# Performance work log

Hardware: AMD Instinct MI355X
Metric: run time of the kernel (lower is better)

The kernel has to match this reference:

```python
import jax, jax.numpy as jnp
import numpy as np

ALPHA = 0.2  # leaky relu slope
NEG = -1e9


def setup_inputs() -> dict:
    key = jax.random.key(0)
    ks = jax.random.split(key, 8)
    B, N, F_IN, H, HID, OUT = 2, 4096, 512, 4, 128, 64
    x = jax.random.normal(ks[0], (B, N, F_IN), dtype=jnp.float32)
    adj = jax.random.randint(ks[1], (B, N, N), 0, 2, dtype=jnp.int32)
    s_in = float(np.sqrt(2.0 / (F_IN + HID)))
    W_heads = jax.random.normal(ks[2], (H, HID, F_IN), dtype=jnp.float32) * s_in
    a1_heads = jax.random.normal(ks[3], (H, HID), dtype=jnp.float32) * 0.1
    a2_heads = jax.random.normal(ks[4], (H, HID), dtype=jnp.float32) * 0.1
    s_out = float(np.sqrt(2.0 / (H * HID + OUT)))
    W_out = jax.random.normal(ks[5], (OUT, H * HID), dtype=jnp.float32) * s_out
    a1_out = jax.random.normal(ks[6], (OUT,), dtype=jnp.float32) * 0.1
    a2_out = jax.random.normal(ks[7], (OUT,), dtype=jnp.float32) * 0.1
    return {"x": x, "adj": adj, "W_heads": W_heads, "a1_heads": a1_heads,
            "a2_heads": a2_heads, "W_out": W_out, "a1_out": a1_out, "a2_out": a2_out}


def _gat_layer(x, adj, W, a1, a2, concat):
    # x: [B,N,F], W: [O,F], a1/a2: [O]
    h = jnp.einsum('bnf,of->bno', x, W)            # [B,N,O]
    f1 = jnp.einsum('bno,o->bn', h, a1)            # [B,N]
    f2 = jnp.einsum('bno,o->bn', h, a2)            # [B,N]
    e = f1[:, :, None] + f2[:, None, :]            # [B,N,N] additive scores
    e = jnp.where(e > 0, e, ALPHA * e)             # leaky relu
    e = jnp.where(adj == 0, NEG, e)                # adjacency mask
    att = jax.nn.softmax(e, axis=2)
    h_prime = jnp.einsum('bnm,bmo->bno', att, h)
    return jax.nn.elu(h_prime) if concat else h_prime


def reference(x, adj, W_heads, a1_heads, a2_heads, W_out, a1_out, a2_out):
    H = W_heads.shape[0]
    heads = [_gat_layer(x, adj, W_heads[i], a1_heads[i], a2_heads[i], True)
             for i in range(H)]
    x_cat = jnp.concatenate(heads, axis=2)         # [B,N,H*HID]
    return _gat_layer(x_cat, adj, W_out, a1_out, a2_out, False)
```

## Files before the change

### kernel.cpp

```cpp
#include <hip/hip_runtime.h>

#define TB 2
#define TN 4096
#define TH 4
#define THID 128
#define TOUT 64
#define NW 128

using f4    = __attribute__((ext_vector_type(4))) float;
using s16x8 = __attribute__((ext_vector_type(8))) short;
using s16x4 = __attribute__((ext_vector_type(4))) short;
using u32x4 = __attribute__((ext_vector_type(4))) unsigned;

static __device__ __forceinline__ short f2bf(float f){
  unsigned u = __float_as_uint(f);
  unsigned r = u + 0x7FFFu + ((u >> 16) & 1u);
  return (short)(r >> 16);
}
static __device__ __forceinline__ float bf2f(short s){
  return __uint_as_float(((unsigned)(unsigned short)s) << 16);
}
static __device__ __forceinline__ unsigned encf(float f){
  unsigned u = __float_as_uint(f);
  return (u & 0x80000000u) ? ~u : (u | 0x80000000u);
}
static __device__ __forceinline__ float decf(unsigned u){
  unsigned v = (u & 0x80000000u) ? (u & 0x7FFFFFFFu) : ~u;
  return __uint_as_float(v);
}
static __device__ __forceinline__ void gll16(const void* g, void* l){
  __builtin_amdgcn_global_load_lds((const __attribute__((address_space(1))) unsigned int*)g,
                                   (__attribute__((address_space(3))) unsigned int*)l, 16, 0, 0);
}
static __device__ __forceinline__ f4 mfma_bf16(s16x8 a, s16x8 b, f4 c){
  return __builtin_amdgcn_mfma_f32_16x16x32_bf16(a, b, c, 0, 0, 0);
}

__global__ void k_pack(const int* __restrict__ adj, unsigned* __restrict__ adjp,
                       unsigned* __restrict__ mx){
  if (blockIdx.x == 0 && threadIdx.x < 16) mx[threadIdx.x] = 0;
  int t = blockIdx.x * 256 + threadIdx.x;
  const int4* p = (const int4*)adj + (size_t)t * 8;
  unsigned m = 0;
#pragma unroll
  for (int i = 0; i < 8; ++i){
    int4 v = p[i];
    m |= (v.x != 0 ? 1u : 0u) << (i*4+0);
    m |= (v.y != 0 ? 1u : 0u) << (i*4+1);
    m |= (v.z != 0 ? 1u : 0u) << (i*4+2);
    m |= (v.w != 0 ? 1u : 0u) << (i*4+3);
  }
  adjp[t] = m;
}

__global__ void k_split(const float* __restrict__ x, short* __restrict__ hi, short* __restrict__ lo){
  int t = blockIdx.x * 256 + threadIdx.x;
  f4 v = ((const f4*)x)[t];
  s16x4 h, l;
#pragma unroll
  for (int e = 0; e < 4; ++e){
    short hb = f2bf(v[e]);
    h[e] = hb;
    l[e] = f2bf(v[e] - bf2f(hb));
  }
  ((s16x4*)hi)[t] = h;
  ((s16x4*)lo)[t] = l;
}
__global__ void k_cvt(const float* __restrict__ x, short* __restrict__ o){
  int t = blockIdx.x * 256 + threadIdx.x;
  f4 v = ((const f4*)x)[t];
  s16x4 h;
#pragma unroll
  for (int e = 0; e < 4; ++e) h[e] = f2bf(v[e]);
  ((s16x4*)o)[t] = h;
}

__global__ __launch_bounds__(512, 2) void k_gemm1(
    const short* __restrict__ xh, const short* __restrict__ xl,
    const short* __restrict__ wh, const short* __restrict__ wl,
    const float* __restrict__ a1h, const float* __restrict__ a2h,
    short* __restrict__ hTb, float* __restrict__ f1g,
    float* __restrict__ Qa, float* __restrict__ Sa, unsigned* __restrict__ mx){
  __shared__ short tiles[2][4][8192];
  __shared__ float red[2][128][2];
  __shared__ float bmx[2];
  int tid = threadIdx.x, lane = tid & 63, w = tid >> 6;
  int kgrp = lane >> 4, li = lane & 15;
  int nblk = blockIdx.x >> 6, mblk = blockIdx.x & 63;
  int n0 = nblk * 128, m0 = mblk * 128;
  int wn = w >> 2, wm = w & 3;
  const f4 fz = {0.f, 0.f, 0.f, 0.f};
  f4 acc[4][2];
#pragma unroll
  for (int i = 0; i < 4; ++i)
#pragma unroll
    for (int j = 0; j < 2; ++j) acc[i][j] = fz;

#pragma unroll
  for (int tno = 0; tno < 4; ++tno){
    const short* gb = (tno==0 ? wh : tno==1 ? wl : tno==2 ? xh : xl);
    int r0 = (tno < 2) ? n0 : m0;
#pragma unroll
    for (int i = 0; i < 2; ++i){
      int s = (i*8 + w)*64 + lane;
      int row = s >> 3, c = s & 7, cs = c ^ (row & 7);
      gll16(gb + (size_t)(r0 + row)*512 + cs*8, (char*)tiles[0][tno] + (i*8+w)*1024);
    }
  }
  asm volatile("s_waitcnt vmcnt(0)" ::: "memory");
  __syncthreads();

  for (int kt = 0; kt < 8; ++kt){
    int cur = kt & 1;
    if (kt < 7){
      int k0 = (kt+1) * 64;
#pragma unroll
      for (int tno = 0; tno < 4; ++tno){
        const short* gb = (tno==0 ? wh : tno==1 ? wl : tno==2 ? xh : xl);
        int r0 = (tno < 2) ? n0 : m0;
#pragma unroll
        for (int i = 0; i < 2; ++i){
          int s = (i*8 + w)*64 + lane;
          int row = s >> 3, c = s & 7, cs = c ^ (row & 7);
          gll16(gb + (size_t)(r0 + row)*512 + k0 + cs*8, (char*)tiles[cur^1][tno] + (i*8+w)*1024);
        }
      }
    }
    const char* t0 = (const char*)tiles[cur][0];
    const char* t1 = (const char*)tiles[cur][1];
    const char* t2 = (const char*)tiles[cur][2];
    const char* t3 = (const char*)tiles[cur][3];
#pragma unroll
    for (int ks = 0; ks < 2; ++ks){
      int ck = ks*4 + kgrp;
      s16x8 ah[4], al[4], bh[2], bl[2];
#pragma unroll
      for (int fn = 0; fn < 4; ++fn){
        int row = wn*64 + fn*16 + li;
        int off = row*128 + ((ck ^ (row & 7)) << 4);
        ah[fn] = *(const s16x8*)(t0 + off);
        al[fn] = *(const s16x8*)(t1 + off);
      }
#pragma unroll
      for (int fm = 0; fm < 2; ++fm){
        int row = wm*32 + fm*16 + li;
        int off = row*128 + ((ck ^ (row & 7)) << 4);
        bh[fm] = *(const s16x8*)(t2 + off);
        bl[fm] = *(const s16x8*)(t3 + off);
      }
#pragma unroll
      for (int fn = 0; fn < 4; ++fn)
#pragma unroll
        for (int fm = 0; fm < 2; ++fm)
          acc[fn][fm] = mfma_bf16(ah[fn], bh[fm], acc[fn][fm]);
#pragma unroll
      for (int fn = 0; fn < 4; ++fn)
#pragma unroll
        for (int fm = 0; fm < 2; ++fm)
          acc[fn][fm] = mfma_bf16(ah[fn], bl[fm], acc[fn][fm]);
#pragma unroll
      for (int fn = 0; fn < 4; ++fn)
#pragma unroll
        for (int fm = 0; fm < 2; ++fm)
          acc[fn][fm] = mfma_bf16(al[fn], bh[fm], acc[fn][fm]);
    }
    asm volatile("s_waitcnt vmcnt(0)" ::: "memory");
    __syncthreads();
  }
  int head = nblk;
#pragma unroll
  for (int fn = 0; fn < 4; ++fn){
#pragma unroll
    for (int fm = 0; fm < 2; ++fm){
#pragma unroll
      for (int r = 0; r < 4; ++r){
        int nout = n0 + wn*64 + fn*16 + kgrp*4 + r;
        int m = m0 + wm*32 + fm*16 + li;
        int b = m >> 12, n = m & 4095;
        int hid = nout & 127;
        size_t idx = ((size_t)((b*TH + head)*THID + hid))*TN + n;
        hTb[idx] = f2bf(acc[fn][fm][r]);
      }
    }
  }
  const float* a1p = a1h + head*THID;
  const float* a2p = a2h + head*THID;
  float s1[2] = {0.f, 0.f}, s2[2] = {0.f, 0.f};
#pragma unroll
  for (int fn = 0; fn < 4; ++fn)
#pragma unroll
    for (int r = 0; r < 4; ++r){
      int row = wn*64 + fn*16 + kgrp*4 + r;
      float w1 = a1p[row], w2 = a2p[row];
#pragma unroll
      for (int fm = 0; fm < 2; ++fm){
        s1[fm] = fmaf(acc[fn][fm][r], w1, s1[fm]);
        s2[fm] = fmaf(acc[fn][fm][r], w2, s2[fm]);
      }
    }
#pragma unroll
  for (int fm = 0; fm < 2; ++fm){
    s1[fm] += __shfl_xor(s1[fm], 16); s1[fm] += __shfl_xor(s1[fm], 32);
    s2[fm] += __shfl_xor(s2[fm], 16); s2[fm] += __shfl_xor(s2[fm], 32);
  }
  if (kgrp == 0){
#pragma unroll
    for (int fm = 0; fm < 2; ++fm){
      int col = wm*32 + fm*16 + li;
      red[wn][col][0] = s1[fm];
      red[wn][col][1] = s2[fm];
    }
  }
  __syncthreads();
  if (tid < 128){
    float f1v = red[0][tid][0] + red[1][tid][0];
    float f2v = red[0][tid][1] + red[1][tid][1];
    int m = m0 + tid, b = m >> 12, n = m & 4095;
    int idx = (b*TH + head)*TN + n;
    f1g[idx] = f1v;
    Qa[idx] = expf(f2v);
    Sa[idx] = expf(0.2f*f2v);
    float wmx = f2v;
#pragma unroll
    for (int d = 1; d < 64; d <<= 1) wmx = fmaxf(wmx, __shfl_xor(wmx, d));
    if ((tid & 63) == 0) bmx[tid >> 6] = wmx;
  }
  __syncthreads();
  if (tid == 0){
    int b = m0 >> 12;
    atomicMax(&mx[b*TH + head], encf(fmaxf(bmx[0], bmx[1])));
  }
}

__global__ __launch_bounds__(256, 4) void k_attn1(
    const short* __restrict__ hTb, const float* __restrict__ f1,
    const float* __restrict__ Qa, const float* __restrict__ Sa,
    const unsigned* __restrict__ adjp, const unsigned* __restrict__ mx,
    short* __restrict__ part, float* __restrict__ sums){
  __shared__ short tile[2][8192];
  __shared__ float Qs[1024], Ss[1024];
  int tid = threadIdx.x, lane = tid & 63, w = tid >> 6;
  int kgrp = lane >> 4, li = lane & 15;
  int bid = blockIdx.x;
  int js = bid >> 8, b = (bid >> 7) & 1, h = (bid >> 5) & 3, rblk = bid & 31;
  int bh = b*TH + h;
  int jbase = js * 1024;
  const short* hbase = hTb + ((size_t)bh*THID)*TN;

  gll16(Qa + (size_t)bh*TN + jbase + w*256 + lane*4, (char*)Qs + w*1024);
  gll16(Sa + (size_t)bh*TN + jbase + w*256 + lane*4, (char*)Ss + w*1024);
#pragma unroll
  for (int i = 0; i < 4; ++i){
    int s = (i*4 + w)*64 + lane;
    int row = s >> 3, c = s & 7, cs = c ^ (row & 7);
    gll16(hbase + (size_t)row*TN + jbase + cs*8, (char*)tile[0] + (i*4+w)*1024);
  }
  int r0 = rblk*128 + w*32;
  float Pv[2], Rv[2];
  int rowa[2];
  float mf = decf(mx[bh]);
#pragma unroll
  for (int rf = 0; rf < 2; ++rf){
    int row = r0 + rf*16 + li;
    rowa[rf] = row;
    float f1v = f1[bh*TN + row];
    float e = f1v + mf;
    float m = e > 0.f ? e : 0.2f*e;
    Pv[rf] = expf(f1v - m);
    Rv[rf] = expf(0.2f*f1v - m);
  }
  const f4 fz = {0.f,0.f,0.f,0.f};
  f4 acc[2][8];
#pragma unroll
  for (int i = 0; i < 2; ++i)
#pragma unroll
    for (int j = 0; j < 8; ++j) acc[i][j] = fz;
  f4 accs[2] = {fz, fz};
  s16x8 ones;
#pragma unroll
  for (int e = 0; e < 8; ++e) ones[e] = (short)0x3F80;

  uint2 awc[2], awn[2];
#pragma unroll
  for (int rf = 0; rf < 2; ++rf)
    awc[rf] = *(const uint2*)&adjp[(size_t)(b*TN + rowa[rf])*NW + (jbase >> 5)];

  asm volatile("s_waitcnt vmcnt(0)" ::: "memory");
  __syncthreads();

  for (int jt = 0; jt < 16; ++jt){
    int cur = jt & 1;
    if (jt < 15){
      int jg = jbase + (jt+1)*64;
#pragma unroll
      for (int i = 0; i < 4; ++i){
        int s = (i*4 + w)*64 + lane;
        int row = s >> 3, c = s & 7, cs = c ^ (row & 7);
        gll16(hbase + (size_t)row*TN + jg + cs*8, (char*)tile[cur^1] + (i*4+w)*1024);
      }
    }
    int jn = jt < 15 ? jt+1 : jt;
#pragma unroll
    for (int rf = 0; rf < 2; ++rf)
      awn[rf] = *(const uint2*)&adjp[(size_t)(b*TN + rowa[rf])*NW + ((jbase + jn*64) >> 5)];
    int j0 = jt*64;
    const char* tp = (const char*)tile[cur];
#pragma unroll
    for (int ks = 0; ks < 2; ++ks){
      int jloc = j0 + ks*32 + kgrp*8;
      float qv[8], sv[8];
      *(f4*)&qv[0] = *(const f4*)&Qs[jloc];
      *(f4*)&qv[4] = *(const f4*)&Qs[jloc+4];
      *(f4*)&sv[0] = *(const f4*)&Ss[jloc];
      *(f4*)&sv[4] = *(const f4*)&Ss[jloc+4];
      s16x8 af[2];
#pragma unroll
      for (int rf = 0; rf < 2; ++rf){
        unsigned word = ks ? awc[rf].y : awc[rf].x;
        unsigned byt = (word >> (kgrp*8)) & 0xFFu;
        float P = Pv[rf], R = Rv[rf];
        u32x4 pw;
#pragma unroll
        for (int pe = 0; pe < 4; ++pe){
          float va = fmaxf(P*qv[2*pe],   R*sv[2*pe]);
          float vb = fmaxf(P*qv[2*pe+1], R*sv[2*pe+1]);
          va = (byt & (1u << (2*pe)))   ? va : 0.f;
          vb = (byt & (1u << (2*pe+1))) ? vb : 0.f;
          unsigned ua = __float_as_uint(va) + 0x8000u;
          unsigned ub = __float_as_uint(vb) + 0x8000u;
          pw[pe] = __builtin_amdgcn_perm(ub, ua, 0x07060302);
        }
        af[rf] = __builtin_bit_cast(s16x8, pw);
      }
      accs[0] = mfma_bf16(af[0], ones, accs[0]);
      accs[1] = mfma_bf16(af[1], ones, accs[1]);
#pragma unroll
      for (int cf = 0; cf < 8; ++cf){
        int col = cf*16 + li;
        int off = col*128 + (((ks*4 + kgrp) ^ (col & 7)) << 4);
        s16x8 bfr = *(const s16x8*)(tp + off);
        acc[0][cf] = mfma_bf16(af[0], bfr, acc[0][cf]);
        acc[1][cf] = mfma_bf16(af[1], bfr, acc[1][cf]);
      }
    }
    asm volatile("s_waitcnt vmcnt(0)" ::: "memory");
    __syncthreads();
    awc[0] = awn[0]; awc[1] = awn[1];
  }
  int sl = js*8 + bh;
  if (li == 0){
#pragma unroll
    for (int rf = 0; rf < 2; ++rf)
#pragma unroll
      for (int r = 0; r < 4; ++r)
        sums[(size_t)sl*TN + r0 + rf*16 + kgrp*4 + r] = accs[rf][r];
  }
#pragma unroll
  for (int rf = 0; rf < 2; ++rf)
#pragma unroll
    for (int cf = 0; cf < 8; ++cf)
#pragma unroll
      for (int r = 0; r < 4; ++r){
        int row = r0 + rf*16 + kgrp*4 + r;
        int hid = cf*16 + li;
        part[((size_t)sl*TN + row)*THID + hid] = f2bf(acc[rf][cf][r]);
      }
}

__global__ void k_comb1(const short* __restrict__ part, const float* __restrict__ sums,
                        short* __restrict__ xcat){
  int t = blockIdx.x*256 + threadIdx.x;
  int hid8 = t & 15, n = (t >> 4) & 4095, h = (t >> 16) & 3, b = t >> 18;
  int bh = b*TH + h;
  float a[8] = {0,0,0,0,0,0,0,0};
  float s = 0.f;
#pragma unroll
  for (int js = 0; js < 4; ++js){
    size_t rowoff = (size_t)(js*8 + bh)*TN + n;
    s16x8 pv = *(const s16x8*)(part + rowoff*THID + hid8*8);
#pragma unroll
    for (int e = 0; e < 8; ++e) a[e] += bf2f(pv[e]);
    s += sums[rowoff];
  }
  float inv = 1.f / s;
  s16x8 o;
#pragma unroll
  for (int e = 0; e < 8; ++e){
    float x = a[e] * inv;
    o[e] = f2bf(x > 0.f ? x : expm1f(x));
  }
  *(s16x8*)(xcat + ((size_t)(b*TN + n))*512 + h*128 + hid8*8) = o;
}

__global__ __launch_bounds__(128) void k_gemm2(
    const short* __restrict__ xcat, const short* __restrict__ wo,
    const float* __restrict__ a1o, const float* __restrict__ a2o,
    short* __restrict__ h2T, float* __restrict__ f1o,
    float* __restrict__ Q2, float* __restrict__ S2, unsigned* __restrict__ mx2){
  int tid = threadIdx.x, lane = tid & 63, w = tid >> 6;
  int kgrp = lane >> 4, li = lane & 15;
  int m0 = blockIdx.x * 32;
  const f4 fz = {0.f,0.f,0.f,0.f};
  f4 acc[4] = {fz, fz, fz, fz};
  int rowA = m0 + w*16 + li;
  for (int kt = 0; kt < 16; ++kt){
    int k = kt*32 + kgrp*8;
    s16x8 a = *(const s16x8*)(xcat + (size_t)rowA*512 + k);
#pragma unroll
    for (int cf = 0; cf < 4; ++cf){
      int col = cf*16 + li;
      s16x8 bfr = *(const s16x8*)(wo + (size_t)col*512 + k);
      acc[cf] = mfma_bf16(a, bfr, acc[cf]);
    }
  }
  float p1[4] = {0,0,0,0}, p2[4] = {0,0,0,0};
#pragma unroll
  for (int cf = 0; cf < 4; ++cf){
    int o = cf*16 + li;
    float w1 = a1o[o], w2 = a2o[o];
#pragma unroll
    for (int r = 0; r < 4; ++r){
      p1[r] = fmaf(acc[cf][r], w1, p1[r]);
      p2[r] = fmaf(acc[cf][r], w2, p2[r]);
    }
  }
#pragma unroll
  for (int r = 0; r < 4; ++r){
#pragma unroll
    for (int d = 1; d < 16; d <<= 1){
      p1[r] += __shfl_xor(p1[r], d);
      p2[r] += __shfl_xor(p2[r], d);
    }
  }
#pragma unroll
  for (int cf = 0; cf < 4; ++cf)
#pragma unroll
    for (int r = 0; r < 4; ++r){
      int row = m0 + w*16 + kgrp*4 + r;
      int o = cf*16 + li;
      int b = row >> 12, n = row & 4095;
      h2T[((size_t)(b*TOUT + o))*TN + n] = f2bf(acc[cf][r]);
    }
  if (li == 0){
#pragma unroll
    for (int r = 0; r < 4; ++r){
      int row = m0 + w*16 + kgrp*4 + r;
      f1o[row] = p1[r];
      Q2[row] = expf(p2[r]);
      S2[row] = expf(0.2f*p2[r]);
    }
  }
  float m2 = fmaxf(fmaxf(p2[0], p2[1]), fmaxf(p2[2], p2[3]));
  m2 = fmaxf(m2, __shfl_xor(m2, 16));
  m2 = fmaxf(m2, __shfl_xor(m2, 32));
  __shared__ float bm[2];
  if (lane == 0) bm[w] = m2;
  __syncthreads();
  if (tid == 0) atomicMax(&mx2[m0 >> 12], encf(fmaxf(bm[0], bm[1])));
}

__global__ __launch_bounds__(256, 4) void k_attn2(
    const short* __restrict__ h2T, const float* __restrict__ f1o,
    const float* __restrict__ Q2, const float* __restrict__ S2,
    const unsigned* __restrict__ adjp, const unsigned* __restrict__ mx2,
    float* __restrict__ part, float* __restrict__ sums){
  __shared__ short tile[2][4096];
  __shared__ float Qs[512], Ss[512];
  int tid = threadIdx.x, lane = tid & 63, w = tid >> 6;
  int kgrp = lane >> 4, li = lane & 15;
  int bid = blockIdx.x;
  int js = bid >> 7, b = (bid >> 6) & 1, rblk = bid & 63;
  int jbase = js * 512;
  const short* hbase = h2T + (size_t)b*TOUT*TN;

  if (w < 2) gll16(Q2 + (size_t)b*TN + jbase + w*256 + lane*4, (char*)Qs + w*1024);
  else       gll16(S2 + (size_t)b*TN + jbase + (w-2)*256 + lane*4, (char*)Ss + (w-2)*1024);
#pragma unroll
  for (int i = 0; i < 2; ++i){
    int s = (i*4 + w)*64 + lane;
    int row = s >> 3, c = s & 7, cs = c ^ (row & 7);
    gll16(hbase + (size_t)row*TN + jbase + cs*8, (char*)tile[0] + (i*4+w)*1024);
  }
  int r0 = rblk*64 + w*16;
  int rowa = r0 + li;
  float mf = decf(mx2[b]);
  float f1v = f1o[b*TN + rowa];
  float e0 = f1v + mf;
  float m0v = e0 > 0.f ? e0 : 0.2f*e0;
  float Pv = expf(f1v - m0v);
  float Rv = expf(0.2f*f1v - m0v);
  const f4 fz = {0.f,0.f,0.f,0.f};
  f4 acc[4] = {fz, fz, fz, fz};
  f4 accs = fz;
  s16x8 ones;
#pragma unroll
  for (int e = 0; e < 8; ++e) ones[e] = (short)0x3F80;

  uint2 awc, awn;
  awc = *(const uint2*)&adjp[(size_t)(b*TN + rowa)*NW + (jbase >> 5)];

  asm volatile("s_waitcnt vmcnt(0)" ::: "memory");
  __syncthreads();

  for (int jt = 0; jt < 8; ++jt){
    int cur = jt & 1;
    if (jt < 7){
      int jg = jbase + (jt+1)*64;
#pragma unroll
      for (int i = 0; i < 2; ++i){
        int s = (i*4 + w)*64 + lane;
        int row = s >> 3, c = s & 7, cs = c ^ (row & 7);
        gll16(hbase + (size_t)row*TN + jg + cs*8, (char*)tile[cur^1] + (i*4+w)*1024);
      }
    }
    int jn = jt < 7 ? jt+1 : jt;
    awn = *(const uint2*)&adjp[(size_t)(b*TN + rowa)*NW + ((jbase + jn*64) >> 5)];
    int j0 = jt*64;
    const char* tp = (const char*)tile[cur];
#pragma unroll
    for (int ks = 0; ks < 2; ++ks){
      int jloc = j0 + ks*32 + kgrp*8;
      float qv[8], sv[8];
      *(f4*)&qv[0] = *(const f4*)&Qs[jloc];
      *(f4*)&qv[4] = *(const f4*)&Qs[jloc+4];
      *(f4*)&sv[0] = *(const f4*)&Ss[jloc];
      *(f4*)&sv[4] = *(const f4*)&Ss[jloc+4];
      unsigned word = ks ? awc.y : awc.x;
      unsigned byt = (word >> (kgrp*8)) & 0xFFu;
      u32x4 pw;
#pragma unroll
      for (int pe = 0; pe < 4; ++pe){
        float va = fmaxf(Pv*qv[2*pe],   Rv*sv[2*pe]);
        float vb = fmaxf(Pv*qv[2*pe+1], Rv*sv[2*pe+1]);
        va = (byt & (1u << (2*pe)))   ? va : 0.f;
        vb = (byt & (1u << (2*pe+1))) ? vb : 0.f;
        unsigned ua = __float_as_uint(va) + 0x8000u;
        unsigned ub = __float_as_uint(vb) + 0x8000u;
        pw[pe] = __builtin_amdgcn_perm(ub, ua, 0x07060302);
      }
      s16x8 af = __builtin_bit_cast(s16x8, pw);
      accs = mfma_bf16(af, ones, accs);
#pragma unroll
      for (int cf = 0; cf < 4; ++cf){
        int col = cf*16 + li;
        int off = col*128 + (((ks*4 + kgrp) ^ (col & 7)) << 4);
        s16x8 bfr = *(const s16x8*)(tp + off);
        acc[cf] = mfma_bf16(af, bfr, acc[cf]);
      }
    }
    asm volatile("s_waitcnt vmcnt(0)" ::: "memory");
    __syncthreads();
    awc = awn;
  }
  int sl = js*2 + b;
  if (li == 0){
#pragma unroll
    for (int r = 0; r < 4; ++r)
      sums[(size_t)sl*TN + r0 + kgrp*4 + r] = accs[r];
  }
#pragma unroll
  for (int cf = 0; cf < 4; ++cf)
#pragma unroll
    for (int r = 0; r < 4; ++r){
      int row = r0 + kgrp*4 + r;
      int o = cf*16 + li;
      part[((size_t)sl*TN + row)*TOUT + o] = acc[cf][r];
    }
}

__global__ void k_comb2(const float* __restrict__ part, const float* __restrict__ sums,
                        float* __restrict__ out){
  int t = blockIdx.x*256 + threadIdx.x;
  int o4 = t & 15, n = (t >> 4) & 4095, b = t >> 16;
  f4 a = {0.f,0.f,0.f,0.f};
  float s = 0.f;
#pragma unroll
  for (int js = 0; js < 8; ++js){
    int sl = js*2 + b;
    a += ((const f4*)part)[((size_t)sl*TN + n)*16 + o4];
    s += sums[(size_t)sl*TN + n];
  }
  f4 r = a / s;
  ((f4*)out)[((size_t)(b*TN + n))*16 + o4] = r;
}

extern "C" void kernel_launch(void* const* d_in, const int* in_sizes, int n_in,
                              void* d_out, int out_size, void* d_ws, size_t ws_size,
                              hipStream_t stream) {
  (void)in_sizes; (void)n_in; (void)out_size; (void)ws_size;
  const float* x       = (const float*)d_in[0];
  const int*   adj     = (const int*)d_in[1];
  const float* W_heads = (const float*)d_in[2];
  const float* a1h     = (const float*)d_in[3];
  const float* a2h     = (const float*)d_in[4];
  const float* W_out   = (const float*)d_in[5];
  const float* a1o     = (const float*)d_in[6];
  const float* a2o     = (const float*)d_in[7];

  char* p = (char*)d_ws;
  auto alloc = [&](size_t sz){ char* r = p; p += (sz + 255) & ~(size_t)255; return r; };
  unsigned* adjp  = (unsigned*) alloc(4ull*1048576);
  short*    wo    = (short*)    alloc(2ull*32768);
  short*    hTb   = (short*)    alloc(2ull*4194304);
  float*    f1    = (float*)    alloc(4ull*32768);
  float*    Qa    = (float*)    alloc(4ull*32768);
  float*    Sa    = (float*)    alloc(4ull*32768);
  unsigned* mx    = (unsigned*) alloc(4ull*16);
  short*    xcat  = (short*)    alloc(2ull*4194304);
  float*    f1o   = (float*)    alloc(4ull*8192);
  float*    Q2    = (float*)    alloc(4ull*8192);
  float*    S2    = (float*)    alloc(4ull*8192);
  short*    h2T   = (short*)    alloc(2ull*524288);
  float*    sums1 = (float*)    alloc(4ull*131072);
  float*    sums2 = (float*)    alloc(4ull*65536);
  char* A = alloc(33554432ull);
  short* xh   = (short*)A;
  short* xl   = (short*)(A + 8388608);
  short* part1 = (short*)A;
  char* Bu = alloc(16777216ull);
  short* wh = (short*)Bu;
  short* wl = (short*)(Bu + 524288);
  float* part2 = (float*)Bu;

  k_pack <<<4096, 256, 0, stream>>>(adj, adjp, mx);
  k_split<<<4096, 256, 0, stream>>>(x, xh, xl);
  k_split<<<256, 256, 0, stream>>>(W_heads, wh, wl);
  k_cvt  <<<32, 256, 0, stream>>>(W_out, wo);
  k_gemm1<<<256, 512, 0, stream>>>(xh, xl, wh, wl, a1h, a2h, hTb, f1, Qa, Sa, mx);
  k_attn1<<<1024, 256, 0, stream>>>(hTb, f1, Qa, Sa, adjp, mx, part1, sums1);
  k_comb1<<<2048, 256, 0, stream>>>(part1, sums1, xcat);
  k_gemm2<<<256, 128, 0, stream>>>(xcat, wo, a1o, a2o, h2T, f1o, Q2, S2, mx + 8);
  k_attn2<<<1024, 256, 0, stream>>>(h2T, f1o, Q2, S2, adjp, mx + 8, part2, sums2);
  k_comb2<<<512, 256, 0, stream>>>(part2, sums2, (float*)d_out);
}
```

Before: 154.5 us.

## Transpose packed adjacency and deepen attention pipelines to four LDS stages

The packed adjacency bitmask is now stored transposed (word-major, node-minor), so each attention tile's mask bits can be bulk-loaded into LDS with global_load_lds alongside the feature tile. Both attention kernels move from a double-buffered loop with a full vmcnt(0) wait and barrier per step to a four-buffer ring with three tiles in flight and partial vmcnt waits. The second-layer attention now covers 1024 columns per block with half the blocks, so the final combine reduces over fewer splits. Occupancy hints drop to fit the larger LDS footprint, and the pack kernel's global reads become strided across rows, which may cost some bandwidth.

```diff
diff --git a/kernel.cpp b/kernel.cpp
--- a/kernel.cpp
+++ b/kernel.cpp
@@ -36,11 +36,12 @@
   return __builtin_amdgcn_mfma_f32_16x16x32_bf16(a, b, c, 0, 0, 0);
 }
 
-__global__ void k_pack(const int* __restrict__ adj, unsigned* __restrict__ adjp,
+__global__ void k_pack(const int* __restrict__ adj, unsigned* __restrict__ adjT,
                        unsigned* __restrict__ mx){
   if (blockIdx.x == 0 && threadIdx.x < 16) mx[threadIdx.x] = 0;
   int t = blockIdx.x * 256 + threadIdx.x;
-  const int4* p = (const int4*)adj + (size_t)t * 8;
+  int n = t & 4095, w = (t >> 12) & 127, b = t >> 19;
+  const int4* p = (const int4*)(adj + ((size_t)(b*TN + n))*TN + w*32);
   unsigned m = 0;
 #pragma unroll
   for (int i = 0; i < 8; ++i){
@@ -50,7 +51,7 @@
     m |= (v.z != 0 ? 1u : 0u) << (i*4+2);
     m |= (v.w != 0 ? 1u : 0u) << (i*4+3);
   }
-  adjp[t] = m;
+  adjT[((size_t)(b*NW + w))*TN + n] = m;
 }
 
 __global__ void k_split(const float* __restrict__ x, short* __restrict__ hi, short* __restrict__ lo){
@@ -232,37 +233,50 @@
   }
 }
 
-__global__ __launch_bounds__(256, 4) void k_attn1(
+__global__ __launch_bounds__(256, 2) void k_attn1(
     const short* __restrict__ hTb, const float* __restrict__ f1,
     const float* __restrict__ Qa, const float* __restrict__ Sa,
-    const unsigned* __restrict__ adjp, const unsigned* __restrict__ mx,
+    const unsigned* __restrict__ adjT, const unsigned* __restrict__ mx,
     short* __restrict__ part, float* __restrict__ sums){
-  __shared__ short tile[2][8192];
+  __shared__ short tile[4][8192];
   __shared__ float Qs[1024], Ss[1024];
+  __shared__ unsigned abuf[4][256];
   int tid = threadIdx.x, lane = tid & 63, w = tid >> 6;
   int kgrp = lane >> 4, li = lane & 15;
   int bid = blockIdx.x;
   int js = bid >> 8, b = (bid >> 7) & 1, h = (bid >> 5) & 3, rblk = bid & 31;
   int bh = b*TH + h;
   int jbase = js * 1024;
+  int r0b = rblk * 128;
   const short* hbase = hTb + ((size_t)bh*THID)*TN;
-
-  gll16(Qa + (size_t)bh*TN + jbase + w*256 + lane*4, (char*)Qs + w*1024);
-  gll16(Sa + (size_t)bh*TN + jbase + w*256 + lane*4, (char*)Ss + w*1024);
-#pragma unroll
-  for (int i = 0; i < 4; ++i){
-    int s = (i*4 + w)*64 + lane;
-    int row = s >> 3, c = s & 7, cs = c ^ (row & 7);
-    gll16(hbase + (size_t)row*TN + jbase + cs*8, (char*)tile[0] + (i*4+w)*1024);
-  }
-  int r0 = rblk*128 + w*32;
+  const float* Qrow = Qa + (size_t)bh*TN + jbase;
+  const float* Srow = Sa + (size_t)bh*TN + jbase;
+
+  auto STAGE = [&](int t){
+    int jg = jbase + t*64;
+    char* dst = (char*)tile[t & 3];
+#pragma unroll
+    for (int i = 0; i < 4; ++i){
+      int s = (i*4 + w)*64 + lane;
+      int row = s >> 3, c = s & 7, cs = c ^ (row & 7);
+      gll16(hbase + (size_t)row*TN + jg + cs*8, dst + (i*4+w)*1024);
+    }
+    int w0 = jg >> 5;
+    gll16(adjT + (size_t)(b*NW + w0 + (lane>>5))*TN + r0b + (lane&31)*4, (char*)abuf[t & 3]);
+  };
+
+  gll16(Qrow + w*256 + lane*4, (char*)Qs + w*1024);
+  gll16(Srow + w*256 + lane*4, (char*)Ss + w*1024);
+  STAGE(0); STAGE(1); STAGE(2);
+
+  int r0 = r0b + w*32;
   float Pv[2], Rv[2];
-  int rowa[2];
+  int lrow[2];
   float mf = decf(mx[bh]);
 #pragma unroll
   for (int rf = 0; rf < 2; ++rf){
     int row = r0 + rf*16 + li;
-    rowa[rf] = row;
+    lrow[rf] = w*32 + rf*16 + li;
     float f1v = f1[bh*TN + row];
     float e = f1v + mf;
     float m = e > 0.f ? e : 0.2f*e;
@@ -280,31 +294,23 @@
 #pragma unroll
   for (int e = 0; e < 8; ++e) ones[e] = (short)0x3F80;
 
-  uint2 awc[2], awn[2];
-#pragma unroll
-  for (int rf = 0; rf < 2; ++rf)
-    awc[rf] = *(const uint2*)&adjp[(size_t)(b*TN + rowa[rf])*NW + (jbase >> 5)];
-
-  asm volatile("s_waitcnt vmcnt(0)" ::: "memory");
-  __syncthreads();
-
   for (int jt = 0; jt < 16; ++jt){
-    int cur = jt & 1;
-    if (jt < 15){
-      int jg = jbase + (jt+1)*64;
-#pragma unroll
-      for (int i = 0; i < 4; ++i){
-        int s = (i*4 + w)*64 + lane;
-        int row = s >> 3, c = s & 7, cs = c ^ (row & 7);
-        gll16(hbase + (size_t)row*TN + jg + cs*8, (char*)tile[cur^1] + (i*4+w)*1024);
-      }
-    }
-    int jn = jt < 15 ? jt+1 : jt;
-#pragma unroll
-    for (int rf = 0; rf < 2; ++rf)
-      awn[rf] = *(const uint2*)&adjp[(size_t)(b*TN + rowa[rf])*NW + ((jbase + jn*64) >> 5)];
+    if (jt < 14)       asm volatile("s_waitcnt vmcnt(10)" ::: "memory");
+    else if (jt == 14) asm volatile("s_waitcnt vmcnt(5)" ::: "memory");
+    else               asm volatile("s_waitcnt vmcnt(0)" ::: "memory");
+    __builtin_amdgcn_s_barrier();
+    __builtin_amdgcn_sched_barrier(0);
+    if (jt < 13) STAGE(jt + 3);
+
     int j0 = jt*64;
-    const char* tp = (const char*)tile[cur];
+    const char* tp = (const char*)tile[jt & 3];
+    const unsigned* ab = abuf[jt & 3];
+    unsigned aw0[2], aw1[2];
+#pragma unroll
+    for (int rf = 0; rf < 2; ++rf){
+      aw0[rf] = ab[lrow[rf]];
+      aw1[rf] = ab[128 + lrow[rf]];
+    }
 #pragma unroll
     for (int ks = 0; ks < 2; ++ks){
       int jloc = j0 + ks*32 + kgrp*8;
@@ -316,7 +322,7 @@
       s16x8 af[2];
 #pragma unroll
       for (int rf = 0; rf < 2; ++rf){
-        unsigned word = ks ? awc[rf].y : awc[rf].x;
+        unsigned word = ks ? aw1[rf] : aw0[rf];
         unsigned byt = (word >> (kgrp*8)) & 0xFFu;
         float P = Pv[rf], R = Rv[rf];
         u32x4 pw;
@@ -343,9 +349,6 @@
         acc[1][cf] = mfma_bf16(af[1], bfr, acc[1][cf]);
       }
     }
-    asm volatile("s_waitcnt vmcnt(0)" ::: "memory");
-    __syncthreads();
-    awc[0] = awn[0]; awc[1] = awn[1];
   }
   int sl = js*8 + bh;
   if (li == 0){
@@ -459,32 +462,46 @@
   if (tid == 0) atomicMax(&mx2[m0 >> 12], encf(fmaxf(bm[0], bm[1])));
 }
 
-__global__ __launch_bounds__(256, 4) void k_attn2(
+__global__ __launch_bounds__(256, 3) void k_attn2(
     const short* __restrict__ h2T, const float* __restrict__ f1o,
     const float* __restrict__ Q2, const float* __restrict__ S2,
-    const unsigned* __restrict__ adjp, const unsigned* __restrict__ mx2,
+    const unsigned* __restrict__ adjT, const unsigned* __restrict__ mx2,
     float* __restrict__ part, float* __restrict__ sums){
-  __shared__ short tile[2][4096];
-  __shared__ float Qs[512], Ss[512];
+  __shared__ short tile[4][4096];
+  __shared__ float Qs[1024], Ss[1024];
+  __shared__ unsigned abuf[4][128];
   int tid = threadIdx.x, lane = tid & 63, w = tid >> 6;
   int kgrp = lane >> 4, li = lane & 15;
   int bid = blockIdx.x;
   int js = bid >> 7, b = (bid >> 6) & 1, rblk = bid & 63;
-  int jbase = js * 512;
+  int jbase = js * 1024;
+  int r0b = rblk * 64;
   const short* hbase = h2T + (size_t)b*TOUT*TN;
-
-  if (w < 2) gll16(Q2 + (size_t)b*TN + jbase + w*256 + lane*4, (char*)Qs + w*1024);
-  else       gll16(S2 + (size_t)b*TN + jbase + (w-2)*256 + lane*4, (char*)Ss + (w-2)*1024);
-#pragma unroll
-  for (int i = 0; i < 2; ++i){
-    int s = (i*4 + w)*64 + lane;
-    int row = s >> 3, c = s & 7, cs = c ^ (row & 7);
-    gll16(hbase + (size_t)row*TN + jbase + cs*8, (char*)tile[0] + (i*4+w)*1024);
-  }
-  int r0 = rblk*64 + w*16;
-  int rowa = r0 + li;
+  const float* Qrow = Q2 + (size_t)b*TN + jbase;
+  const float* Srow = S2 + (size_t)b*TN + jbase;
+
+  auto STAGE = [&](int t){
+    int jg = jbase + t*64;
+    char* dst = (char*)tile[t & 3];
+#pragma unroll
+    for (int i = 0; i < 2; ++i){
+      int s = (i*4 + w)*64 + lane;
+      int row = s >> 3, c = s & 7, cs = c ^ (row & 7);
+      gll16(hbase + (size_t)row*TN + jg + cs*8, dst + (i*4+w)*1024);
+    }
+    int w0 = jg >> 5;
+    if (lane < 32)
+      gll16(adjT + (size_t)(b*NW + w0 + (lane>>4))*TN + r0b + (lane&15)*4, (char*)abuf[t & 3]);
+  };
+
+  gll16(Qrow + w*256 + lane*4, (char*)Qs + w*1024);
+  gll16(Srow + w*256 + lane*4, (char*)Ss + w*1024);
+  STAGE(0); STAGE(1); STAGE(2);
+
+  int r0 = r0b + w*16;
+  int lrow = w*16 + li;
   float mf = decf(mx2[b]);
-  float f1v = f1o[b*TN + rowa];
+  float f1v = f1o[b*TN + r0 + li];
   float e0 = f1v + mf;
   float m0v = e0 > 0.f ? e0 : 0.2f*e0;
   float Pv = expf(f1v - m0v);
@@ -496,27 +513,18 @@
 #pragma unroll
   for (int e = 0; e < 8; ++e) ones[e] = (short)0x3F80;
 
-  uint2 awc, awn;
-  awc = *(const uint2*)&adjp[(size_t)(b*TN + rowa)*NW + (jbase >> 5)];
-
-  asm volatile("s_waitcnt vmcnt(0)" ::: "memory");
-  __syncthreads();
-
-  for (int jt = 0; jt < 8; ++jt){
-    int cur = jt & 1;
-    if (jt < 7){
-      int jg = jbase + (jt+1)*64;
-#pragma unroll
-      for (int i = 0; i < 2; ++i){
-        int s = (i*4 + w)*64 + lane;
-        int row = s >> 3, c = s & 7, cs = c ^ (row & 7);
-        gll16(hbase + (size_t)row*TN + jg + cs*8, (char*)tile[cur^1] + (i*4+w)*1024);
-      }
-    }
-    int jn = jt < 7 ? jt+1 : jt;
-    awn = *(const uint2*)&adjp[(size_t)(b*TN + rowa)*NW + ((jbase + jn*64) >> 5)];
+  for (int jt = 0; jt < 16; ++jt){
+    if (jt < 14)       asm volatile("s_waitcnt vmcnt(6)" ::: "memory");
+    else if (jt == 14) asm volatile("s_waitcnt vmcnt(3)" ::: "memory");
+    else               asm volatile("s_waitcnt vmcnt(0)" ::: "memory");
+    __builtin_amdgcn_s_barrier();
+    __builtin_amdgcn_sched_barrier(0);
+    if (jt < 13) STAGE(jt + 3);
+
     int j0 = jt*64;
-    const char* tp = (const char*)tile[cur];
+    const char* tp = (const char*)tile[jt & 3];
+    const unsigned* ab = abuf[jt & 3];
+    unsigned aw0 = ab[lrow], aw1 = ab[64 + lrow];
 #pragma unroll
     for (int ks = 0; ks < 2; ++ks){
       int jloc = j0 + ks*32 + kgrp*8;
@@ -525,7 +533,7 @@
       *(f4*)&qv[4] = *(const f4*)&Qs[jloc+4];
       *(f4*)&sv[0] = *(const f4*)&Ss[jloc];
       *(f4*)&sv[4] = *(const f4*)&Ss[jloc+4];
-      unsigned word = ks ? awc.y : awc.x;
+      unsigned word = ks ? aw1 : aw0;
       unsigned byt = (word >> (kgrp*8)) & 0xFFu;
       u32x4 pw;
 #pragma unroll
@@ -548,9 +556,6 @@
         acc[cf] = mfma_bf16(af, bfr, acc[cf]);
       }
     }
-    asm volatile("s_waitcnt vmcnt(0)" ::: "memory");
-    __syncthreads();
-    awc = awn;
   }
   int sl = js*2 + b;
   if (li == 0){
@@ -575,7 +580,7 @@
   f4 a = {0.f,0.f,0.f,0.f};
   float s = 0.f;
 #pragma unroll
-  for (int js = 0; js < 8; ++js){
+  for (int js = 0; js < 4; ++js){
     int sl = js*2 + b;
     a += ((const f4*)part)[((size_t)sl*TN + n)*16 + o4];
     s += sums[(size_t)sl*TN + n];
@@ -599,7 +604,7 @@
 
   char* p = (char*)d_ws;
   auto alloc = [&](size_t sz){ char* r = p; p += (sz + 255) & ~(size_t)255; return r; };
-  unsigned* adjp  = (unsigned*) alloc(4ull*1048576);
+  unsigned* adjT  = (unsigned*) alloc(4ull*1048576);
   short*    wo    = (short*)    alloc(2ull*32768);
   short*    hTb   = (short*)    alloc(2ull*4194304);
   float*    f1    = (float*)    alloc(4ull*32768);
@@ -622,14 +627,14 @@
   short* wl = (short*)(Bu + 524288);
   float* part2 = (float*)Bu;
 
-  k_pack <<<4096, 256, 0, stream>>>(adj, adjp, mx);
+  k_pack <<<4096, 256, 0, stream>>>(adj, adjT, mx);
   k_split<<<4096, 256, 0, stream>>>(x, xh, xl);
   k_split<<<256, 256, 0, stream>>>(W_heads, wh, wl);
   k_cvt  <<<32, 256, 0, stream>>>(W_out, wo);
   k_gemm1<<<256, 512, 0, stream>>>(xh, xl, wh, wl, a1h, a2h, hTb, f1, Qa, Sa, mx);
-  k_attn1<<<1024, 256, 0, stream>>>(hTb, f1, Qa, Sa, adjp, mx, part1, sums1);
+  k_attn1<<<1024, 256, 0, stream>>>(hTb, f1, Qa, Sa, adjT, mx, part1, sums1);
   k_comb1<<<2048, 256, 0, stream>>>(part1, sums1, xcat);
   k_gemm2<<<256, 128, 0, stream>>>(xcat, wo, a1o, a2o, h2T, f1o, Q2, S2, mx + 8);
-  k_attn2<<<1024, 256, 0, stream>>>(h2T, f1o, Q2, S2, adjp, mx + 8, part2, sums2);
+  k_attn2<<<512, 256, 0, stream>>>(h2T, f1o, Q2, S2, adjT, mx + 8, part2, sums2);
   k_comb2<<<512, 256, 0, stream>>>(part2, sums2, (float*)d_out);
 }
```

New measurement: 153.6 us. Within noise of the previous version (-0.5%).
